# Optimization experiments

Measured on AMD Instinct MI355X. Metric: run time of the kernel, lower is better.

The kernel has to match this reference:

```python
import jax, jax.numpy as jnp
import numpy as np

B, S, T = 16, 256, 256
E, H = 1024, 512          # embedded_size = 2*hidden_size (required by the module's math)
ENV, ZHV = 32000, 32000


def gru_layer(x, h0, Wih, Whh, bih, bhh):
    # x: [B,T,in], h0: [B,H]; PyTorch GRU cell semantics
    xp = jnp.einsum('bti,gi->btg', x, Wih) + bih  # precompute input projections [B,T,3H]

    def step(h, xp_t):
        hp = h @ Whh.T + bhh
        xr, xz, xn = jnp.split(xp_t, 3, axis=-1)
        hr, hz, hn = jnp.split(hp, 3, axis=-1)
        r = jax.nn.sigmoid(xr + hr)
        z = jax.nn.sigmoid(xz + hz)
        n = jnp.tanh(xn + r * hn)
        h_new = (1.0 - z) * n + z * h
        return h_new, h_new

    h_last, ys = jax.lax.scan(step, h0, jnp.swapaxes(xp, 0, 1))
    return jnp.swapaxes(ys, 0, 1), h_last


def gru2(x, h0, p0, p1):
    # 2-layer stacked GRU; h0: [2,B,H]
    y0, h0f = gru_layer(x, h0[0], *p0)
    y1, h1f = gru_layer(y0, h0[1], *p1)
    return y1, jnp.stack([h0f, h1f])


def setup_inputs() -> dict:
    key = jax.random.key(0)
    ks = jax.random.split(key, 32)
    s = 0.05
    f = jnp.float32
    inp = {}
    inp['en_sen'] = jax.random.randint(ks[0], (B, S), 0, ENV)
    inp['zh_sen'] = jax.random.randint(ks[1], (B, T), 0, ZHV)
    inp['en_emb'] = (jax.random.normal(ks[2], (ENV, E)) * s).astype(f)
    inp['zh_emb'] = (jax.random.normal(ks[3], (ZHV, E)) * s).astype(f)
    inp['h0'] = jax.random.normal(ks[4], (2, B, H)).astype(f)
    i = 5
    for tag, in0 in (('e', E), ('d', E)):
        for layer, ind in ((0, in0), (1, H)):
            inp[f'Wih_{tag}{layer}'] = (jax.random.normal(ks[i], (3 * H, ind)) * s).astype(f); i += 1
            inp[f'Whh_{tag}{layer}'] = (jax.random.normal(ks[i], (3 * H, H)) * s).astype(f); i += 1
            inp[f'bih_{tag}{layer}'] = jnp.zeros((3 * H,), f)
            inp[f'bhh_{tag}{layer}'] = jnp.zeros((3 * H,), f)
    inp['fcW'] = (jax.random.normal(ks[i], (ZHV, E)) * s).astype(f)
    inp['fcb'] = jnp.zeros((ZHV,), f)
    return inp


def reference(en_sen, zh_sen, en_emb, zh_emb, h0,
              Wih_e0, Whh_e0, bih_e0, bhh_e0, Wih_e1, Whh_e1, bih_e1, bhh_e1,
              Wih_d0, Whh_d0, bih_d0, bhh_d0, Wih_d1, Whh_d1, bih_d1, bhh_d1,
              fcW, fcb):
    # encoder
    ex = en_emb[en_sen]                                     # [B,S,E]
    en_out, hid = gru2(ex, h0, (Wih_e0, Whh_e0, bih_e0, bhh_e0),
                       (Wih_e1, Whh_e1, bih_e1, bhh_e1))    # [B,S,H], [2,B,H]
    # shift target right with SOS token (zh_vocab_size - 2)
    sos = jnp.full((B, 1), ZHV - 2, dtype=zh_sen.dtype)
    zh = jnp.concatenate([sos, zh_sen[:, :-1]], axis=1)
    zx = zh_emb[zh]                                         # [B,T,E]
    # decoder (teacher forcing = 1.0 -> full-sequence scan is exact)
    dec_out, _ = gru2(zx, hid, (Wih_d0, Whh_d0, bih_d0, bhh_d0),
                      (Wih_d1, Whh_d1, bih_d1, bhh_d1))     # [B,T,H]
    # dot-product attention over encoder states, per decoder timestep
    scores = jnp.einsum('bsh,bth->bst', en_out, dec_out)    # [B,S,T]
    attn = jax.nn.softmax(scores, axis=1)                   # softmax over source dim
    ctx = jnp.einsum('bst,bsh->bth', attn, en_out)          # [B,T,H]
    de = jnp.concatenate([dec_out, ctx], axis=-1)           # [B,T,2H] == [B,T,E]
    out = de.reshape(-1, E) @ fcW.T + fcb                   # [B*T, ZHV]
    return out
```

## Files before the change

### kernel.cpp

```cpp
#include <hip/hip_runtime.h>
#include <math.h>

#define B_ 16
#define S_ 256
#define T_ 256
#define E_ 1024
#define H_ 512
#define G_ 1536
#define V_ 32000

typedef unsigned short u16;
typedef unsigned int u32;
typedef short short8 __attribute__((ext_vector_type(8)));
typedef short short4v __attribute__((ext_vector_type(4)));
typedef float f32x4 __attribute__((ext_vector_type(4)));

__device__ inline u16 f2bf(float x) {
  union { float f; unsigned u; } a; a.f = x;
  unsigned r = a.u + 0x7fff + ((a.u >> 16) & 1);
  return (u16)(r >> 16);
}
__device__ inline void split2(float x, u16& hi, u16& lo) {
  union { float f; unsigned u; } a; a.f = x;
  hi = (u16)(a.u >> 16);
  union { unsigned u; float f; } b; b.u = a.u & 0xffff0000u;
  lo = f2bf(x - b.f);
}

__device__ inline f32x4 load_f4_coh(const float* p) {
  f32x4 v;
  asm volatile("global_load_dwordx4 %0, %1, off sc0 sc1" : "=v"(v) : "v"(p));
  return v;
}

__device__ inline float dot4(f32x4 a, f32x4 b) {
  return a.x * b.x + a.y * b.y + a.z * b.z + a.w * b.w;
}

__global__ __launch_bounds__(256) void k_embed_enc(const int* __restrict__ sen,
                                                   const float* __restrict__ emb,
                                                   float* __restrict__ out) {
  long row = blockIdx.x;
  int tid = threadIdx.x;
  long e = sen[row];
  float4 v = *(const float4*)(emb + e * E_ + tid * 4);
  *(float4*)(out + row * E_ + tid * 4) = v;
}

__global__ __launch_bounds__(256) void k_embed_dec(const int* __restrict__ zh,
                                                   const float* __restrict__ emb,
                                                   float* __restrict__ out) {
  long row = blockIdx.x;
  int b = (int)(row >> 8), t = (int)(row & 255);
  int tid = threadIdx.x;
  long e = (t == 0) ? (V_ - 2) : zh[b * T_ + t - 1];
  float4 v = *(const float4*)(emb + e * E_ + tid * 4);
  *(float4*)(out + row * E_ + tid * 4) = v;
}

__global__ __launch_bounds__(256) void k_transpose(const float* __restrict__ in,
                                                   float* __restrict__ out, int R, int C) {
  __shared__ float tile[32][33];
  long z = blockIdx.z;
  const float* inz = in + z * (long)R * C;
  float* outz = out + z * (long)R * C;
  int x = blockIdx.x * 32 + threadIdx.x;
  int y0 = blockIdx.y * 32;
#pragma unroll
  for (int i = threadIdx.y; i < 32; i += 8)
    tile[i][threadIdx.x] = inz[(long)(y0 + i) * C + x];
  __syncthreads();
  int xo = y0 + threadIdx.x;
#pragma unroll
  for (int i = threadIdx.y; i < 32; i += 8) {
    int yo = blockIdx.x * 32 + i;
    outz[(long)yo * R + xo] = tile[threadIdx.x][i];
  }
}

__global__ __launch_bounds__(256) void k_gemm_nt(
    const float* __restrict__ A, int lda, const float* __restrict__ A2, int lda2, int kSplit,
    const float* __restrict__ Bm, int ldb, const float* __restrict__ bias,
    float* __restrict__ C, int ldc, int K, long sA, long sB, long sC) {
  __shared__ float As[8][132];
  __shared__ float Bs[8][132];
  int z = blockIdx.z;
  A += z * sA;
  Bm += z * sB;
  C += z * sC;
  int tid = threadIdx.x;
  int bm = blockIdx.y * 128, bn = blockIdx.x * 128;
  int tx = tid & 15, ty = tid >> 4;
  int lr = tid >> 1, lc = (tid & 1) * 4;
  float acc[8][8] = {};
  for (int k0 = 0; k0 < K; k0 += 8) {
    int ka = k0 + lc;
    const float* ap;
    if (A2 != nullptr && ka >= kSplit)
      ap = A2 + (long)(bm + lr) * lda2 + (ka - kSplit);
    else
      ap = A + (long)(bm + lr) * lda + ka;
    float4 a4 = *(const float4*)ap;
    float4 b4 = *(const float4*)(Bm + (long)(bn + lr) * ldb + k0 + lc);
    As[lc + 0][lr] = a4.x; As[lc + 1][lr] = a4.y; As[lc + 2][lr] = a4.z; As[lc + 3][lr] = a4.w;
    Bs[lc + 0][lr] = b4.x; Bs[lc + 1][lr] = b4.y; Bs[lc + 2][lr] = b4.z; Bs[lc + 3][lr] = b4.w;
    __syncthreads();
#pragma unroll
    for (int kk = 0; kk < 8; kk++) {
      float ar[8], br[8];
      *(float4*)&ar[0] = *(const float4*)&As[kk][ty * 8];
      *(float4*)&ar[4] = *(const float4*)&As[kk][ty * 8 + 4];
      *(float4*)&br[0] = *(const float4*)&Bs[kk][tx * 8];
      *(float4*)&br[4] = *(const float4*)&Bs[kk][tx * 8 + 4];
#pragma unroll
      for (int i = 0; i < 8; i++)
#pragma unroll
        for (int j = 0; j < 8; j++) acc[i][j] += ar[i] * br[j];
    }
    __syncthreads();
  }
  float bv[8];
#pragma unroll
  for (int j = 0; j < 8; j++) bv[j] = bias ? bias[bn + tx * 8 + j] : 0.f;
#pragma unroll
  for (int i = 0; i < 8; i++) {
    float* cp = C + (long)(bm + ty * 8 + i) * ldc + bn + tx * 8;
    float4 o0, o1;
    o0.x = acc[i][0] + bv[0]; o0.y = acc[i][1] + bv[1];
    o0.z = acc[i][2] + bv[2]; o0.w = acc[i][3] + bv[3];
    o1.x = acc[i][4] + bv[4]; o1.y = acc[i][5] + bv[5];
    o1.z = acc[i][6] + bv[6]; o1.w = acc[i][7] + bv[7];
    *(float4*)cp = o0;
    *(float4*)(cp + 4) = o1;
  }
}


__global__ __launch_bounds__(256) void k_gemm_mfma_nt(
    const float* __restrict__ A, int lda, const float* __restrict__ A2, int lda2, int kSplit,
    const float* __restrict__ Bm, int ldb, const float* __restrict__ bias,
    float* __restrict__ C, int ldc, int K) {
  __shared__ short8 Ah[512], Al[512], Bh[512], Bl[512];
  int tid = threadIdx.x;
  int bm = blockIdx.y * 128, bn = blockIdx.x * 128;
  int wave = tid >> 6, lane = tid & 63;
  int wm = (wave >> 1) * 64, wn = (wave & 1) * 64;
  int srow = tid >> 1, scol = (tid & 1) * 16, q0 = (tid & 1) * 2;
  int fr = lane & 15, fq = lane >> 4;
  int ua = (srow >> 6) * 256 + ((srow >> 4) & 3) * 64 + q0 * 16 + (srow & 15);
  int abase = (wm >> 6) * 256 + lane;
  int bbase = (wn >> 6) * 256 + lane;

  f32x4 acc[4][4] = {};

  for (int k0 = 0; k0 < K; k0 += 32) {
    {
      int ka = k0 + scol;
      const float* ap;
      if (A2 != nullptr && ka >= kSplit)
        ap = A2 + (long)(bm + srow) * lda2 + (ka - kSplit);
      else
        ap = A + (long)(bm + srow) * lda + ka;
      float va[16];
      *(float4*)&va[0] = *(const float4*)ap;
      *(float4*)&va[4] = *(const float4*)(ap + 4);
      *(float4*)&va[8] = *(const float4*)(ap + 8);
      *(float4*)&va[12] = *(const float4*)(ap + 12);
      u16 h[16], l[16];
#pragma unroll
      for (int i = 0; i < 16; i++) split2(va[i], h[i], l[i]);
      Ah[ua] = *(short8*)&h[0];
      Ah[ua + 16] = *(short8*)&h[8];
      Al[ua] = *(short8*)&l[0];
      Al[ua + 16] = *(short8*)&l[8];
    }
    {
      const float* bp = Bm + (long)(bn + srow) * ldb + k0 + scol;
      float vb[16];
      *(float4*)&vb[0] = *(const float4*)bp;
      *(float4*)&vb[4] = *(const float4*)(bp + 4);
      *(float4*)&vb[8] = *(const float4*)(bp + 8);
      *(float4*)&vb[12] = *(const float4*)(bp + 12);
      u16 h[16], l[16];
#pragma unroll
      for (int i = 0; i < 16; i++) split2(vb[i], h[i], l[i]);
      Bh[ua] = *(short8*)&h[0];
      Bh[ua + 16] = *(short8*)&h[8];
      Bl[ua] = *(short8*)&l[0];
      Bl[ua + 16] = *(short8*)&l[8];
    }
    __syncthreads();
    short8 afh[4], afl[4];
#pragma unroll
    for (int mt = 0; mt < 4; mt++) {
      afh[mt] = Ah[abase + mt * 64];
      afl[mt] = Al[abase + mt * 64];
    }
#pragma unroll
    for (int nt = 0; nt < 4; nt++) {
      short8 bh = Bh[bbase + nt * 64];
      short8 bl = Bl[bbase + nt * 64];
#pragma unroll
      for (int mt = 0; mt < 4; mt++) {
        acc[mt][nt] = __builtin_amdgcn_mfma_f32_16x16x32_bf16(afh[mt], bh, acc[mt][nt], 0, 0, 0);
        acc[mt][nt] = __builtin_amdgcn_mfma_f32_16x16x32_bf16(afh[mt], bl, acc[mt][nt], 0, 0, 0);
        acc[mt][nt] = __builtin_amdgcn_mfma_f32_16x16x32_bf16(afl[mt], bh, acc[mt][nt], 0, 0, 0);
      }
    }
    __syncthreads();
  }
  int fq4 = fq * 4;
#pragma unroll
  for (int nt = 0; nt < 4; nt++) {
    int col = bn + wn + nt * 16 + fr;
    float bv = bias ? bias[col] : 0.f;
#pragma unroll
    for (int mt = 0; mt < 4; mt++) {
      int row = bm + wm + mt * 16 + fq4;
#pragma unroll
      for (int j = 0; j < 4; j++)
        C[(long)(row + j) * ldc + col] = acc[mt][nt][j] + bv;
    }
  }
}

__global__ __launch_bounds__(256) void k_presplit(const float* __restrict__ src,
                                                  u16* __restrict__ hi,
                                                  u16* __restrict__ lo) {
  long i0 = ((long)blockIdx.x * 256 + threadIdx.x) * 8;
  float v[8];
  *(float4*)&v[0] = *(const float4*)(src + i0);
  *(float4*)&v[4] = *(const float4*)(src + i0 + 4);
  u16 h[8], l[8];
#pragma unroll
  for (int i = 0; i < 8; i++) split2(v[i], h[i], l[i]);
  *(short8*)(hi + i0) = *(short8*)&h[0];
  *(short8*)(lo + i0) = *(short8*)&l[0];
}

__global__ __launch_bounds__(256) void k_presplit_cat(const float* __restrict__ a,
                                                      const float* __restrict__ b,
                                                      u16* __restrict__ hi,
                                                      u16* __restrict__ lo) {
  long row = blockIdx.x;
  int tid = threadIdx.x;
  const float* src = (tid < 128) ? (a + row * 512 + tid * 4)
                                 : (b + row * 512 + (tid - 128) * 4);
  float4 v = *(const float4*)src;
  u16 h[4], l[4];
  split2(v.x, h[0], l[0]); split2(v.y, h[1], l[1]);
  split2(v.z, h[2], l[2]); split2(v.w, h[3], l[3]);
  *(short4v*)(hi + row * 1024 + tid * 4) = *(short4v*)&h[0];
  *(short4v*)(lo + row * 1024 + tid * 4) = *(short4v*)&l[0];
}

__global__ __launch_bounds__(256) void k_gemm_bf16p_nt(
    const u16* __restrict__ Ahi, const u16* __restrict__ Alo,
    const u16* __restrict__ Bhi, const u16* __restrict__ Blo,
    const float* __restrict__ bias, float* __restrict__ C, int ldc, int K) {
  __shared__ short8 Ah[512], Al[512], Bh[512], Bl[512];
  int tid = threadIdx.x;
  int bm = blockIdx.y * 128, bn = blockIdx.x * 128;
  int wave = tid >> 6, lane = tid & 63;
  int wm = (wave >> 1) * 64, wn = (wave & 1) * 64;
  int srow = tid >> 1, scol = (tid & 1) * 16, q0 = (tid & 1) * 2;
  int fr = lane & 15, fq = lane >> 4;
  int ua = (srow >> 6) * 256 + ((srow >> 4) & 3) * 64 + q0 * 16 + (srow & 15);
  int abase = (wm >> 6) * 256 + lane;
  int bbase = (wn >> 6) * 256 + lane;

  f32x4 acc[4][4] = {};
  long aoff = (long)(bm + srow) * K + scol;
  long boff = (long)(bn + srow) * K + scol;

  for (int k0 = 0; k0 < K; k0 += 32) {
    short8 ah0 = *(const short8*)(Ahi + aoff + k0);
    short8 ah1 = *(const short8*)(Ahi + aoff + k0 + 8);
    short8 al0 = *(const short8*)(Alo + aoff + k0);
    short8 al1 = *(const short8*)(Alo + aoff + k0 + 8);
    short8 bh0 = *(const short8*)(Bhi + boff + k0);
    short8 bh1 = *(const short8*)(Bhi + boff + k0 + 8);
    short8 bl0 = *(const short8*)(Blo + boff + k0);
    short8 bl1 = *(const short8*)(Blo + boff + k0 + 8);
    Ah[ua] = ah0; Ah[ua + 16] = ah1;
    Al[ua] = al0; Al[ua + 16] = al1;
    Bh[ua] = bh0; Bh[ua + 16] = bh1;
    Bl[ua] = bl0; Bl[ua + 16] = bl1;
    __syncthreads();
    short8 afh[4], afl[4];
#pragma unroll
    for (int mt = 0; mt < 4; mt++) {
      afh[mt] = Ah[abase + mt * 64];
      afl[mt] = Al[abase + mt * 64];
    }
#pragma unroll
    for (int nt = 0; nt < 4; nt++) {
      short8 bh = Bh[bbase + nt * 64];
      short8 bl = Bl[bbase + nt * 64];
#pragma unroll
      for (int mt = 0; mt < 4; mt++) {
        acc[mt][nt] = __builtin_amdgcn_mfma_f32_16x16x32_bf16(afh[mt], bh, acc[mt][nt], 0, 0, 0);
        acc[mt][nt] = __builtin_amdgcn_mfma_f32_16x16x32_bf16(afh[mt], bl, acc[mt][nt], 0, 0, 0);
        acc[mt][nt] = __builtin_amdgcn_mfma_f32_16x16x32_bf16(afl[mt], bh, acc[mt][nt], 0, 0, 0);
      }
    }
    __syncthreads();
  }
  int fq4 = fq * 4;
#pragma unroll
  for (int nt = 0; nt < 4; nt++) {
    int col = bn + wn + nt * 16 + fr;
    float bv = bias ? bias[col] : 0.f;
#pragma unroll
    for (int mt = 0; mt < 4; mt++) {
      int row = bm + wm + mt * 16 + fq4;
#pragma unroll
      for (int j = 0; j < 4; j++)
        C[(long)(row + j) * ldc + col] = acc[mt][nt][j] + bv;
    }
  }
}

#define WSLOT 32
__global__ __launch_bounds__(256) void k_gru_b(
    const float* __restrict__ xp, float* __restrict__ y,
    const float* __restrict__ Whh, const float* __restrict__ bhh,
    const float* __restrict__ hinit, long hbs, int* __restrict__ ep) {
  __shared__ float hls[536];
  int tid = threadIdx.x;
  int wave = tid >> 6, lane = tid & 63;
  int jsub = lane >> 5, ksl = lane & 31;
  int b = blockIdx.x >> 4, js = blockIdx.x & 15;
  int jbase = js * 32 + wave * 8 + jsub * 4;

  f32x4 w[4][3][4];
  float bb[4][3];
#pragma unroll
  for (int e = 0; e < 4; e++)
#pragma unroll
    for (int g = 0; g < 3; g++) {
      const float* r = Whh + (long)(g * 512 + jbase + e) * 512 + ksl * 16;
#pragma unroll
      for (int q = 0; q < 4; q++) w[e][g][q] = *(const f32x4*)(r + q * 4);
      bb[e][g] = bhh[g * 512 + jbase + e];
    }
  bool gl = (ksl < 4);
  int jme = jbase + ksl;
  const int* epb = ep + (long)(b * 16 + (lane & 15)) * WSLOT;
  int* epMine = ep + (long)(b * 16 + js) * WSLOT;
  float* yb = y + (long)b * (256 * 512);
  const float* xpb = xp + (long)b * (256 * 1536);

  for (int t = 0; t < 256; t++) {
    float xr = 0.f, xz = 0.f, xn = 0.f;
    if (gl) {
      const float* xpt = xpb + (long)t * 1536 + jme;
      xr = xpt[0]; xz = xpt[512]; xn = xpt[1024];
    }
    if (t > 0) {
      if (wave == 0) {
        while (true) {
          int e0;
          asm volatile("global_load_dword %0, %1, off sc0 sc1" : "=v"(e0) : "v"(epb));
          asm volatile("s_waitcnt vmcnt(0)" ::: "memory");
          if (__ballot(e0 >= t) == ~0ull) break;
          __builtin_amdgcn_s_sleep(1);
        }
      }
      __syncthreads();
    }
    if (tid < 128) {
      const float* src = (t == 0) ? (hinit + (long)b * hbs + tid * 4)
                                  : (yb + (long)(t - 1) * 512 + tid * 4);
      f32x4 v = load_f4_coh(src);
      asm volatile("s_waitcnt vmcnt(0)" ::: "memory");
      __builtin_amdgcn_sched_barrier(0);
      *(f32x4*)&hls[(tid & 3) * 132 + (tid >> 2) * 4] = v;
    }
    __syncthreads();
    f32x4 h0 = *(const f32x4*)&hls[ksl * 4];
    f32x4 h1 = *(const f32x4*)&hls[132 + ksl * 4];
    f32x4 h2 = *(const f32x4*)&hls[264 + ksl * 4];
    f32x4 h3 = *(const f32x4*)&hls[396 + ksl * 4];
    float a[4][3];
#pragma unroll
    for (int e = 0; e < 4; e++)
#pragma unroll
      for (int g = 0; g < 3; g++)
        a[e][g] = dot4(h0, w[e][g][0]) + dot4(h1, w[e][g][1]) +
                  dot4(h2, w[e][g][2]) + dot4(h3, w[e][g][3]);
#pragma unroll
    for (int m = 1; m <= 16; m <<= 1)
#pragma unroll
      for (int e = 0; e < 4; e++) {
        a[e][0] += __shfl_xor(a[e][0], m);
        a[e][1] += __shfl_xor(a[e][1], m);
        a[e][2] += __shfl_xor(a[e][2], m);
      }
    if (gl) {
      float hr = 0.f, hz = 0.f, hn = 0.f, Br = 0.f, Bz = 0.f, Bn = 0.f;
#pragma unroll
      for (int e = 0; e < 4; e++)
        if (ksl == e) {
          hr = a[e][0]; hz = a[e][1]; hn = a[e][2];
          Br = bb[e][0]; Bz = bb[e][1]; Bn = bb[e][2];
        }
      float r = 1.f / (1.f + __expf(-(xr + hr + Br)));
      float z = 1.f / (1.f + __expf(-(xz + hz + Bz)));
      float n = tanhf(xn + r * (hn + Bn));
      float hp = hls[((jme >> 2) & 3) * 132 + (jme >> 4) * 4 + (jme & 3)];
      float hv = (1.f - z) * n + z * hp;
      __hip_atomic_store(&yb[(long)t * 512 + jme], hv,
                         __ATOMIC_RELAXED, __HIP_MEMORY_SCOPE_AGENT);
    }
    asm volatile("s_waitcnt vmcnt(0)" ::: "memory");
    __syncthreads();
    if (tid == 0)
      __hip_atomic_store(epMine, t + 1, __ATOMIC_RELAXED, __HIP_MEMORY_SCOPE_AGENT);
  }
}

__global__ __launch_bounds__(256) void k_softmax(float* __restrict__ p) {
  long row = blockIdx.x;
  int tid = threadIdx.x;
  float* pr = p + row * 256;
  float v = pr[tid];
  float m = v;
#pragma unroll
  for (int off = 32; off >= 1; off >>= 1) m = fmaxf(m, __shfl_xor(m, off));
  __shared__ float wmax[4];
  __shared__ float wsum[4];
  int wv = tid >> 6, ln = tid & 63;
  if (ln == 0) wmax[wv] = m;
  __syncthreads();
  m = fmaxf(fmaxf(wmax[0], wmax[1]), fmaxf(wmax[2], wmax[3]));
  float e = expf(v - m);
  float s = e;
#pragma unroll
  for (int off = 32; off >= 1; off >>= 1) s += __shfl_xor(s, off);
  if (ln == 0) wsum[wv] = s;
  __syncthreads();
  s = wsum[0] + wsum[1] + wsum[2] + wsum[3];
  pr[tid] = e / s;
}

extern "C" void kernel_launch(void* const* d_in, const int* in_sizes, int n_in,
                              void* d_out, int out_size, void* d_ws, size_t ws_size,
                              hipStream_t stream) {
  const int* en_sen = (const int*)d_in[0];
  const int* zh_sen = (const int*)d_in[1];
  const float* en_emb = (const float*)d_in[2];
  const float* zh_emb = (const float*)d_in[3];
  const float* h0 = (const float*)d_in[4];
  const float* Wih_e0 = (const float*)d_in[5];
  const float* Whh_e0 = (const float*)d_in[6];
  const float* bih_e0 = (const float*)d_in[7];
  const float* bhh_e0 = (const float*)d_in[8];
  const float* Wih_e1 = (const float*)d_in[9];
  const float* Whh_e1 = (const float*)d_in[10];
  const float* bih_e1 = (const float*)d_in[11];
  const float* bhh_e1 = (const float*)d_in[12];
  const float* Wih_d0 = (const float*)d_in[13];
  const float* Whh_d0 = (const float*)d_in[14];
  const float* bih_d0 = (const float*)d_in[15];
  const float* bhh_d0 = (const float*)d_in[16];
  const float* Wih_d1 = (const float*)d_in[17];
  const float* Whh_d1 = (const float*)d_in[18];
  const float* bih_d1 = (const float*)d_in[19];
  const float* bhh_d1 = (const float*)d_in[20];
  const float* fcW = (const float*)d_in[21];
  const float* fcb = (const float*)d_in[22];
  float* out = (float*)d_out;

  const size_t needFast = (2ull * 32768000 + 2ull * 4194304) * sizeof(u16);
  bool fastFC = (ws_size >= needFast);

  u16* fcWhi = (u16*)d_ws;
  u16* fcWlo = fcWhi + 32768000;
  u16* Ahi = (u16*)(fcWlo + 32768000);
  u16* Alo = Ahi + 4194304;

  int* flags = (int*)d_out;
  float* bufE = (float*)d_out + 32768;
  float* xp = bufE + 4194304;
  float* bufY = xp + 6291456;
  float* enOut = bufY + 2097152;
  float* scT = enOut + 2097152;
  float* enOutT = scT + 1048576;
  float* decOutA = enOutT + 2097152;
  float* ctxA = decOutA + 2097152;

  float* decOut = fastFC ? decOutA : (float*)d_ws;
  float* ctx = fastFC ? ctxA : ((float*)d_ws + 2097152);

  hipMemsetAsync(flags, 0, 32768 * sizeof(int), stream);

  dim3 tb(32, 8);

  if (fastFC)
    k_presplit<<<16000, 256, 0, stream>>>(fcW, fcWhi, fcWlo);

  k_embed_enc<<<B_ * S_, 256, 0, stream>>>(en_sen, en_emb, bufE);
  k_gemm_mfma_nt<<<dim3(G_ / 128, (B_ * S_) / 128, 1), 256, 0, stream>>>(
      bufE, E_, nullptr, 0, E_, Wih_e0, E_, bih_e0, xp, G_, E_);
  k_gru_b<<<256, 256, 0, stream>>>(xp, bufY, Whh_e0, bhh_e0, h0, (long)H_, flags);
  k_gemm_mfma_nt<<<dim3(G_ / 128, (B_ * S_) / 128, 1), 256, 0, stream>>>(
      bufY, H_, nullptr, 0, H_, Wih_e1, H_, bih_e1, xp, G_, H_);
  k_gru_b<<<256, 256, 0, stream>>>(xp, enOut, Whh_e1, bhh_e1, h0 + B_ * H_, (long)H_,
                                   flags + 8192);

  k_embed_dec<<<B_ * T_, 256, 0, stream>>>(zh_sen, zh_emb, bufE);
  k_gemm_mfma_nt<<<dim3(G_ / 128, (B_ * T_) / 128, 1), 256, 0, stream>>>(
      bufE, E_, nullptr, 0, E_, Wih_d0, E_, bih_d0, xp, G_, E_);
  k_gru_b<<<256, 256, 0, stream>>>(xp, bufY, Whh_d0, bhh_d0, bufY + 255 * H_,
                                   (long)(256 * H_), flags + 16384);
  k_gemm_mfma_nt<<<dim3(G_ / 128, (B_ * T_) / 128, 1), 256, 0, stream>>>(
      bufY, H_, nullptr, 0, H_, Wih_d1, H_, bih_d1, xp, G_, H_);
  k_gru_b<<<256, 256, 0, stream>>>(xp, decOut, Whh_d1, bhh_d1, enOut + 255 * H_,
                                   (long)(256 * H_), flags + 24576);

  k_gemm_nt<<<dim3(S_ / 128, T_ / 128, B_), 256, 0, stream>>>(
      decOut, H_, nullptr, 0, H_, enOut, H_, nullptr, scT, S_, H_,
      (long)T_ * H_, (long)S_ * H_, (long)T_ * S_);
  k_softmax<<<B_ * T_, 256, 0, stream>>>(scT);
  k_transpose<<<dim3(16, 8, B_), tb, 0, stream>>>(enOut, enOutT, 256, 512);
  k_gemm_nt<<<dim3(H_ / 128, T_ / 128, B_), 256, 0, stream>>>(
      scT, S_, nullptr, 0, S_, enOutT, S_, nullptr, ctx, H_, S_,
      (long)T_ * S_, (long)H_ * S_, (long)T_ * H_);

  if (fastFC) {
    k_presplit_cat<<<B_ * T_, 256, 0, stream>>>(decOut, ctx, Ahi, Alo);
    k_gemm_bf16p_nt<<<dim3(V_ / 128, (B_ * T_) / 128, 1), 256, 0, stream>>>(
        Ahi, Alo, fcWhi, fcWlo, fcb, out, V_, E_);
  } else {
    k_gemm_mfma_nt<<<dim3(V_ / 128, (B_ * T_) / 128, 1), 256, 0, stream>>>(
        decOut, H_, ctx, H_, H_, fcW, E_, fcb, out, V_, E_);
  }
}
```

Baseline: 4.691 ms.

## XOR-swizzle LDS tiles in MFMA GEMMs and swap FC grid axes

Applies an XOR swizzle to the shared-memory tile indices for both stores and fragment loads in the two split-bf16 MFMA GEMM kernels, aiming to remove LDS bank conflicts. It also swaps the grid dimensions of the big FC GEMM so consecutive blocks walk along M, letting blocks that run at the same time share the same weight tile in cache. The swizzle must match between writers and readers, and the rasterization change alters L2 reuse patterns.

```diff
diff --git a/kernel.cpp b/kernel.cpp
--- a/kernel.cpp
+++ b/kernel.cpp
@@ -147,9 +147,11 @@
   int wm = (wave >> 1) * 64, wn = (wave & 1) * 64;
   int srow = tid >> 1, scol = (tid & 1) * 16, q0 = (tid & 1) * 2;
   int fr = lane & 15, fq = lane >> 4;
-  int ua = (srow >> 6) * 256 + ((srow >> 4) & 3) * 64 + q0 * 16 + (srow & 15);
-  int abase = (wm >> 6) * 256 + lane;
-  int bbase = (wn >> 6) * 256 + lane;
+  int ubase = (srow >> 6) * 256 + ((srow >> 4) & 3) * 64;
+  int ua0 = ubase + q0 * 16 + ((srow & 15) ^ (q0 * 2));
+  int ua1 = ubase + (q0 + 1) * 16 + ((srow & 15) ^ (q0 * 2 + 2));
+  int abase = (wm >> 6) * 256 + fq * 16 + (fr ^ (fq * 2));
+  int bbase = (wn >> 6) * 256 + fq * 16 + (fr ^ (fq * 2));
 
   f32x4 acc[4][4] = {};
 
@@ -169,10 +171,10 @@
       u16 h[16], l[16];
 #pragma unroll
       for (int i = 0; i < 16; i++) split2(va[i], h[i], l[i]);
-      Ah[ua] = *(short8*)&h[0];
-      Ah[ua + 16] = *(short8*)&h[8];
-      Al[ua] = *(short8*)&l[0];
-      Al[ua + 16] = *(short8*)&l[8];
+      Ah[ua0] = *(short8*)&h[0];
+      Ah[ua1] = *(short8*)&h[8];
+      Al[ua0] = *(short8*)&l[0];
+      Al[ua1] = *(short8*)&l[8];
     }
     {
       const float* bp = Bm + (long)(bn + srow) * ldb + k0 + scol;
@@ -184,10 +186,10 @@
       u16 h[16], l[16];
 #pragma unroll
       for (int i = 0; i < 16; i++) split2(vb[i], h[i], l[i]);
-      Bh[ua] = *(short8*)&h[0];
-      Bh[ua + 16] = *(short8*)&h[8];
-      Bl[ua] = *(short8*)&l[0];
-      Bl[ua + 16] = *(short8*)&l[8];
+      Bh[ua0] = *(short8*)&h[0];
+      Bh[ua1] = *(short8*)&h[8];
+      Bl[ua0] = *(short8*)&l[0];
+      Bl[ua1] = *(short8*)&l[8];
     }
     __syncthreads();
     short8 afh[4], afl[4];
@@ -260,14 +262,16 @@
     const float* __restrict__ bias, float* __restrict__ C, int ldc, int K) {
   __shared__ short8 Ah[512], Al[512], Bh[512], Bl[512];
   int tid = threadIdx.x;
-  int bm = blockIdx.y * 128, bn = blockIdx.x * 128;
+  int bm = blockIdx.x * 128, bn = blockIdx.y * 128;
   int wave = tid >> 6, lane = tid & 63;
   int wm = (wave >> 1) * 64, wn = (wave & 1) * 64;
   int srow = tid >> 1, scol = (tid & 1) * 16, q0 = (tid & 1) * 2;
   int fr = lane & 15, fq = lane >> 4;
-  int ua = (srow >> 6) * 256 + ((srow >> 4) & 3) * 64 + q0 * 16 + (srow & 15);
-  int abase = (wm >> 6) * 256 + lane;
-  int bbase = (wn >> 6) * 256 + lane;
+  int ubase = (srow >> 6) * 256 + ((srow >> 4) & 3) * 64;
+  int ua0 = ubase + q0 * 16 + ((srow & 15) ^ (q0 * 2));
+  int ua1 = ubase + (q0 + 1) * 16 + ((srow & 15) ^ (q0 * 2 + 2));
+  int abase = (wm >> 6) * 256 + fq * 16 + (fr ^ (fq * 2));
+  int bbase = (wn >> 6) * 256 + fq * 16 + (fr ^ (fq * 2));
 
   f32x4 acc[4][4] = {};
   long aoff = (long)(bm + srow) * K + scol;
@@ -282,10 +286,10 @@
     short8 bh1 = *(const short8*)(Bhi + boff + k0 + 8);
     short8 bl0 = *(const short8*)(Blo + boff + k0);
     short8 bl1 = *(const short8*)(Blo + boff + k0 + 8);
-    Ah[ua] = ah0; Ah[ua + 16] = ah1;
-    Al[ua] = al0; Al[ua + 16] = al1;
-    Bh[ua] = bh0; Bh[ua + 16] = bh1;
-    Bl[ua] = bl0; Bl[ua + 16] = bl1;
+    Ah[ua0] = ah0; Ah[ua1] = ah1;
+    Al[ua0] = al0; Al[ua1] = al1;
+    Bh[ua0] = bh0; Bh[ua1] = bh1;
+    Bl[ua0] = bl0; Bl[ua1] = bl1;
     __syncthreads();
     short8 afh[4], afl[4];
 #pragma unroll
@@ -530,7 +534,7 @@
 
   if (fastFC) {
     k_presplit_cat<<<B_ * T_, 256, 0, stream>>>(decOut, ctx, Ahi, Alo);
-    k_gemm_bf16p_nt<<<dim3(V_ / 128, (B_ * T_) / 128, 1), 256, 0, stream>>>(
+    k_gemm_bf16p_nt<<<dim3((B_ * T_) / 128, V_ / 128, 1), 256, 0, stream>>>(
         Ahi, Alo, fcWhi, fcWlo, fcb, out, V_, E_);
   } else {
     k_gemm_mfma_nt<<<dim3(V_ / 128, (B_ * T_) / 128, 1), 256, 0, stream>>>(
```

Measured after the change: 4.593 ms. -2.1%, faster.
